# Performance work log

Measured on AMD Instinct MI355X. Metric: run time of the kernel, lower is better.

The kernel has to match this reference:

```python
import jax, jax.numpy as jnp
import numpy as np

K_DIM = 1024
HEADS = 16


def setup_inputs() -> dict:
    key = jax.random.key(0)
    kx, kw1, kb1, kw2, kb2 = jax.random.split(key, 5)
    b, t, k = 4, 2048, K_DIM
    scale = 1.0 / np.sqrt(k)
    x = jax.random.normal(kx, (b, t, k), dtype=jnp.float32)
    # torch nn.Linear params: weight [out, in], bias [out]
    W_qkv = jax.random.normal(kw1, (3 * k, k), dtype=jnp.float32) * scale
    b_qkv = jax.random.normal(kb1, (3 * k,), dtype=jnp.float32) * scale
    W_out = jax.random.normal(kw2, (k, k), dtype=jnp.float32) * scale
    b_out = jax.random.normal(kb2, (k,), dtype=jnp.float32) * scale
    return {"x": x, "W_qkv": W_qkv, "b_qkv": b_qkv, "W_out": W_out, "b_out": b_out}


def reference(x, W_qkv, b_qkv, W_out, b_out):
    b, t, k = x.shape
    h = HEADS
    s = k // h
    # tokqv linear: [b,t,3k]
    kqv = jnp.einsum('btk,ok->bto', x, W_qkv) + b_qkv
    # view [b,t,h,3s] -> transpose -> [b,h,t,3s], then split q,k,v along last dim
    kqv = kqv.reshape(b, t, h, 3 * s).transpose(0, 2, 1, 3)
    q, kk, v = kqv[..., :s], kqv[..., s:2 * s], kqv[..., 2 * s:]
    scores = jnp.einsum('bhqd,bhkd->bhqk', q, kk) / jnp.sqrt(jnp.float32(s * h))  # note: scale uses full k per source (queries.size(-1)=s, but here head dim s)
    # Faithful: original attention scales by sqrt(queries.size(-1)) = sqrt(s)
    scores = jnp.einsum('bhqd,bhkd->bhqk', q, kk) / jnp.sqrt(jnp.float32(s))
    weights = jax.nn.softmax(scores, axis=-1)
    res = jnp.einsum('bhqk,bhkd->bhqd', weights, v)  # [b,h,t,s]
    res = res.transpose(0, 2, 1, 3).reshape(b, t, k)
    return jnp.einsum('btk,ok->bto', res, W_out) + b_out
```

## Files before the change

### kernel.cpp

```cpp
#include <hip/hip_runtime.h>
#include <hip/hip_bf16.h>

typedef float  f32x4  __attribute__((ext_vector_type(4)));
typedef float  f32x8  __attribute__((ext_vector_type(8)));
typedef float  f32x16 __attribute__((ext_vector_type(16)));
typedef __bf16 bf16x8 __attribute__((ext_vector_type(8)));
typedef unsigned short u16x4 __attribute__((ext_vector_type(4)));
typedef unsigned short u16x8 __attribute__((ext_vector_type(8)));
typedef unsigned int   u32x4 __attribute__((ext_vector_type(4)));

#define QSCALE 0.18033688011112042f

__device__ __forceinline__ unsigned short f2bf(float f) {
  __bf16 h = (__bf16)f;
  return __builtin_bit_cast(unsigned short, h);
}

__device__ __forceinline__ f32x4 mfma16(bf16x8 a, bf16x8 b, f32x4 c) {
  return __builtin_amdgcn_mfma_f32_16x16x32_bf16(a, b, c, 0, 0, 0);
}
__device__ __forceinline__ f32x16 mfma32(bf16x8 a, bf16x8 b, f32x16 c) {
  return __builtin_amdgcn_mfma_f32_32x32x16_bf16(a, b, c, 0, 0, 0);
}
__device__ __forceinline__ f32x16 zero16() {
  f32x16 v;
#pragma unroll
  for (int i = 0; i < 16; ++i) v[i] = 0.f;
  return v;
}

typedef const __attribute__((address_space(1))) void* gptr_t;
typedef __attribute__((address_space(3))) void* lptr_t;
__device__ __forceinline__ void gld16(const void* g, void* l) {
  __builtin_amdgcn_global_load_lds((gptr_t)g, (lptr_t)l, 16, 0, 0);
}


__global__ __launch_bounds__(256) void prep_x(const float* __restrict__ x,
                                              unsigned short* __restrict__ A1) {
  const int mb = blockIdx.x >> 5;
  const int kB = blockIdx.x & 31;
#pragma unroll
  for (int ph = 0; ph < 2; ++ph) {
    int c = threadIdx.x + ph * 256;
    int lg = c >> 7, r = c & 127;
    f32x8 v = *(const f32x8*)(x + (size_t)(mb * 128 + r) * 1024 + kB * 32 + lg * 8);
    u16x8 h;
#pragma unroll
    for (int j = 0; j < 8; ++j) h[j] = f2bf(v[j]);
    *(u16x8*)(A1 + (size_t)(mb * 32 + kB) * 4096 + (size_t)c * 8) = h;
  }
}

__global__ __launch_bounds__(256) void prep_w(const float* __restrict__ w,
                                              unsigned short* __restrict__ o) {
  const int rb = blockIdx.x >> 5;
  const int kB = blockIdx.x & 31;
#pragma unroll
  for (int ph = 0; ph < 2; ++ph) {
    int c = threadIdx.x + ph * 256;
    int lg = c >> 7, r = c & 127;
    f32x8 v = *(const f32x8*)(w + (size_t)(rb * 128 + r) * 1024 + kB * 32 + lg * 8);
    u16x8 h;
#pragma unroll
    for (int j = 0; j < 8; ++j) h[j] = f2bf(v[j]);
    *(u16x8*)(o + (size_t)(rb * 32 + kB) * 4096 + (size_t)c * 8) = h;
  }
}

template <int EPI, int MINW>
__global__ __launch_bounds__(256, MINW) void gemm_bt(
    const __bf16* __restrict__ A, const __bf16* __restrict__ B,
    const float* __restrict__ bias, int N, int nbx, int NT,
    unsigned short* __restrict__ q_out, unsigned short* __restrict__ k_out,
    unsigned short* __restrict__ v_out, float* __restrict__ f_out) {
  __shared__ __align__(16) char smem[3 * 16384];
  const int tid = threadIdx.x;
  const int lane = tid & 63;
  const int wave = tid >> 6;
  const int ln = lane & 15, lg = lane >> 4;
  const int wm = wave >> 1;
  const int wn = wave & 1;
  const int bm = blockIdx.x / nbx;
  const int bn = blockIdx.x % nbx;

  f32x4 acc[4][4];
#pragma unroll
  for (int i = 0; i < 4; ++i)
#pragma unroll
    for (int j = 0; j < 4; ++j) acc[i][j] = (f32x4){0.f, 0.f, 0.f, 0.f};

  const __bf16* Asrc = A + ((size_t)bm * NT) * 4096 + tid * 8;
  const __bf16* Bsrc = B + ((size_t)bn * NT) * 4096 + tid * 8;
  const int aoff = lg * 2048 + (wm * 64 + ln) * 16;
  const int boff = 8192 + lg * 2048 + (wn * 64 + ln) * 16;

#define STAGE(slot_, tf_)                                                      \
  do {                                                                         \
    char* d_ = smem + (slot_) * 16384;                                         \
    const __bf16* a_ = Asrc + (size_t)(tf_) * 4096;                            \
    const __bf16* b_ = Bsrc + (size_t)(tf_) * 4096;                            \
    gld16(a_, d_ + tid * 16);                                                  \
    gld16(a_ + 2048, d_ + 4096 + tid * 16);                                    \
    gld16(b_, d_ + 8192 + tid * 16);                                           \
    gld16(b_ + 2048, d_ + 12288 + tid * 16);                                   \
  } while (0)

#define KBODY(t_, scur_, snxt_)                                                \
  do {                                                                         \
    int tf_ = ((t_) + 2 < NT) ? (t_) + 2 : NT - 1;                             \
    STAGE(snxt_, tf_);                                                         \
    const char* ab_ = smem + (scur_) * 16384;                                  \
    bf16x8 af_[4], bq_[4];                                                     \
    _Pragma("unroll") for (int mi = 0; mi < 4; ++mi)                           \
        af_[mi] = *(const bf16x8*)(ab_ + aoff + mi * 256);                     \
    _Pragma("unroll") for (int ni = 0; ni < 4; ++ni)                           \
        bq_[ni] = *(const bf16x8*)(ab_ + boff + ni * 256);                     \
    __builtin_amdgcn_s_setprio(1);                                             \
    _Pragma("unroll") for (int mi = 0; mi < 4; ++mi)                           \
        _Pragma("unroll") for (int ni = 0; ni < 4; ++ni)                       \
            acc[mi][ni] = mfma16(af_[mi], bq_[ni], acc[mi][ni]);               \
    __builtin_amdgcn_s_setprio(0);                                             \
    asm volatile("s_waitcnt vmcnt(4)\n\ts_barrier" ::: "memory");              \
  } while (0)

  STAGE(0, 0);
  STAGE(1, 1);
  asm volatile("s_waitcnt vmcnt(4)\n\ts_barrier" ::: "memory");

  for (int t = 0; t < NT; t += 3) {
    KBODY(t, 0, 2);
    if (t + 1 < NT) KBODY(t + 1, 1, 0);
    if (t + 2 < NT) KBODY(t + 2, 2, 1);
  }
  asm volatile("s_waitcnt vmcnt(0)" ::: "memory");
#undef KBODY
#undef STAGE

#pragma unroll
  for (int mi = 0; mi < 4; ++mi) {
#pragma unroll
    for (int ni = 0; ni < 4; ++ni) {
      int n = bn * 128 + wn * 64 + ni * 16 + ln;
      float bv = bias[n];
#pragma unroll
      for (int j = 0; j < 4; ++j) {
        int m = bm * 128 + wm * 64 + mi * 16 + lg * 4 + j;
        float val = acc[mi][ni][j] + bv;
        if constexpr (EPI == 0) {
          int h = n / 192;
          int r3 = n - h * 192;
          int b = m >> 11;
          int t = m & 2047;
          size_t base = (size_t)(b * 16 + h) << 17;
          if (r3 < 64) {
            q_out[base + ((size_t)t << 6) + r3] = f2bf(val * QSCALE);
          } else if (r3 < 128) {
            int d = r3 - 64;
            size_t off = base + (size_t)(t >> 6) * 4096 +
                         (size_t)((((t >> 5) & 1) << 2) + (d >> 4)) * 512 +
                         ((d >> 3) & 1) * 256 + (t & 31) * 8 + (d & 7);
            k_out[off] = f2bf(val);
          } else {
            int c = r3 - 128;
            size_t off = base + (size_t)(t >> 6) * 4096 +
                         (size_t)(((c >> 5) << 2) + ((t >> 4) & 3)) * 512 +
                         ((t >> 3) & 1) * 256 + (c & 31) * 8 + (t & 7);
            v_out[off] = f2bf(val);
          }
        } else {
          f_out[(size_t)m * N + n] = val;
        }
      }
    }
  }
}

__global__ __launch_bounds__(512, 4) void attn2(
    const __bf16* __restrict__ Q, const __bf16* __restrict__ Kg,
    const __bf16* __restrict__ Vg, unsigned short* __restrict__ res) {
  __shared__ __align__(16) char smem[2 * 32768];
  const int tid = threadIdx.x;
  const int lane = tid & 63;
  const int wq = tid >> 6;
  const int l31 = lane & 31;
  const int hi = lane >> 5;
  const int bh = blockIdx.x & 63;
  const int q0 = (blockIdx.x >> 6) << 8;
  const size_t bh_elem = (size_t)bh << 17;

  const __bf16* Kbh = Kg + bh_elem;
  const __bf16* Vbh = Vg + bh_elem;

  bf16x8 qf[4];
  {
    const __bf16* qrow = Q + bh_elem + ((size_t)(q0 + wq * 32 + l31) << 6) + hi * 8;
#pragma unroll
    for (int ks = 0; ks < 4; ++ks) qf[ks] = *(const bf16x8*)(qrow + ks * 16);
  }
  const u16x8 one8 = {0x3F80, 0x3F80, 0x3F80, 0x3F80,
                      0x3F80, 0x3F80, 0x3F80, 0x3F80};
  const bf16x8 ones = __builtin_bit_cast(bf16x8, one8);

  const f32x16 fz = zero16();
  f32x16 oacc0 = zero16(), oacc1 = zero16(), lacc = zero16();

#define ASTP(s_, p_)                                                           \
  do {                                                                         \
    char* sb_ = smem + (s_) * 32768;                                           \
    const __bf16* k0_ = Kbh + (size_t)(2 * (p_)) * 4096 + tid * 8;             \
    const __bf16* v0_ = Vbh + (size_t)(2 * (p_)) * 4096 + tid * 8;             \
    gld16(k0_, sb_ + tid * 16);                                                \
    gld16(v0_, sb_ + 8192 + tid * 16);                                         \
    gld16(k0_ + 4096, sb_ + 16384 + tid * 16);                                 \
    gld16(v0_ + 4096, sb_ + 24576 + tid * 16);                                 \
  } while (0)

  ASTP(0, 0);
  ASTP(1, 1);
  asm volatile("s_waitcnt vmcnt(4)\n\ts_barrier" ::: "memory");

  const int t2rev = wq & 1;
  for (int pr = 0; pr < 16; ++pr) {
    if (pr >= 1 && pr < 15) ASTP((pr + 1) & 1, pr + 1);

    const char* pbase = smem + (pr & 1) * 32768;
    const int loff = hi * 512 + l31 * 16;

#pragma unroll
    for (int half = 0; half < 2; ++half) {
      const char* kbase = pbase + half * 16384;
      const char* vbase = kbase + 8192;

#pragma unroll
      for (int tt = 0; tt < 2; ++tt) {
        const int t2 = tt ^ t2rev;
        f32x16 s;
        __builtin_amdgcn_s_setprio(1);
        {
          bf16x8 kf0 = *(const bf16x8*)(kbase + (t2 * 4) * 1024 + loff);
          s = mfma32(kf0, qf[0], fz);
        }
#pragma unroll
        for (int ks = 1; ks < 4; ++ks) {
          bf16x8 kf = *(const bf16x8*)(kbase + (t2 * 4 + ks) * 1024 + loff);
          s = mfma32(kf, qf[ks], s);
        }
        __builtin_amdgcn_s_setprio(0);
        float p[16];
#pragma unroll
        for (int r = 0; r < 16; ++r) p[r] = __builtin_amdgcn_exp2f(s[r]);
        unsigned int pk[8];
#pragma unroll
        for (int i = 0; i < 8; ++i)
          pk[i] = ((unsigned int)f2bf(p[2 * i + 1]) << 16) | f2bf(p[2 * i]);
        asm volatile("v_permlane32_swap_b32 %0, %1" : "+v"(pk[0]), "+v"(pk[2]));
        asm volatile("v_permlane32_swap_b32 %0, %1" : "+v"(pk[1]), "+v"(pk[3]));
        asm volatile("v_permlane32_swap_b32 %0, %1" : "+v"(pk[4]), "+v"(pk[6]));
        asm volatile("v_permlane32_swap_b32 %0, %1" : "+v"(pk[5]), "+v"(pk[7]));
        __builtin_amdgcn_s_setprio(1);
#pragma unroll
        for (int ks2 = 0; ks2 < 2; ++ks2) {
          u32x4 bw = {pk[ks2 * 4 + 0], pk[ks2 * 4 + 1],
                      pk[ks2 * 4 + 2], pk[ks2 * 4 + 3]};
          bf16x8 pb = __builtin_bit_cast(bf16x8, bw);
          int kb2 = t2 * 2 + ks2;
          bf16x8 v0 = *(const bf16x8*)(vbase + (kb2) * 1024 + loff);
          bf16x8 v1 = *(const bf16x8*)(vbase + (4 + kb2) * 1024 + loff);
          lacc  = mfma32(ones, pb, lacc);
          oacc0 = mfma32(v0, pb, oacc0);
          oacc1 = mfma32(v1, pb, oacc1);
        }
        __builtin_amdgcn_s_setprio(0);
      }
    }
    asm volatile("s_waitcnt vmcnt(0)\n\ts_barrier" ::: "memory");
  }
#undef ASTP

  float rl = __builtin_amdgcn_rcpf(lacc[0]);
  const int b = bh >> 4, h = bh & 15;
  const int rloc = wq * 32 + l31;
  const int mb = b * 16 + (blockIdx.x >> 6) * 2 + (rloc >> 7);
  const int r = rloc & 127;
  unsigned short* c0 = res + (size_t)(mb * 32 + 2 * h) * 4096 + r * 8 + hi * 4;
#pragma unroll
  for (int g = 0; g < 4; ++g) {
    u16x4 st0, st1;
#pragma unroll
    for (int rr = 0; rr < 4; ++rr) {
      st0[rr] = f2bf(oacc0[g * 4 + rr] * rl);
      st1[rr] = f2bf(oacc1[g * 4 + rr] * rl);
    }
    *(u16x4*)(c0 + g * 1024) = st0;
    *(u16x4*)(c0 + 4096 + g * 1024) = st1;
  }
}

extern "C" void kernel_launch(void* const* d_in, const int* in_sizes, int n_in,
                              void* d_out, int out_size, void* d_ws, size_t ws_size,
                              hipStream_t stream) {
  const float* x    = (const float*)d_in[0];
  const float* Wqkv = (const float*)d_in[1];
  const float* bqkv = (const float*)d_in[2];
  const float* Wout = (const float*)d_in[3];
  const float* bout = (const float*)d_in[4];
  float* out = (float*)d_out;
  char* ws = (char*)d_ws;

  unsigned short* A1 = (unsigned short*)(ws);
  unsigned short* B1 = (unsigned short*)(ws + 50331648);
  unsigned short* Qb = (unsigned short*)(ws + 69206016);
  unsigned short* Kb = (unsigned short*)(ws + 85983232);
  unsigned short* Vb = (unsigned short*)(ws + 102760448);
  unsigned short* Rb = (unsigned short*)(ws + 119537664);
  unsigned short* Wo = (unsigned short*)(ws + 136314880);

  prep_x<<<64 * 32, 256, 0, stream>>>(x, A1);
  prep_w<<<24 * 32, 256, 0, stream>>>(Wqkv, B1);
  prep_w<<<8 * 32, 256, 0, stream>>>(Wout, Wo);

  gemm_bt<0, 3><<<64 * 24, 256, 0, stream>>>((const __bf16*)A1, (const __bf16*)B1,
                                             bqkv, 3072, 24, 32,
                                             Qb, Kb, Vb, nullptr);

  attn2<<<512, 512, 0, stream>>>((const __bf16*)Qb, (const __bf16*)Kb,
                                 (const __bf16*)Vb, Rb);

  gemm_bt<1, 2><<<64 * 8, 256, 0, stream>>>((const __bf16*)Rb, (const __bf16*)Wo,
                                            bout, 1024, 8, 32,
                                            nullptr, nullptr, nullptr, out);
}
```

Before: 180.8 us.

## Restructure GEMM pipeline to double-buffered two-tile stages; use packed bf16 convert

The GEMM main loop changes from a three-slot ring that holds one k-tile per slot to two slots that each hold two k-tiles. Each iteration issues the next pair's loads, computes two k-tiles, then waits for all loads and barriers, so there are half as many barriers per k-step. LDS per block grows to 64 KB and the QKV GEMM launch bound drops from 3 to 2 waves per SIMD, which may lower occupancy and latency hiding. In the attention kernel, packing two floats to bf16 now uses a single v_cvt_pk_bf16_f32 instruction instead of separate converts, shifts and ors.

Result: slower. 185.6 us (+2.7%).

```diff
diff --git a/kernel.cpp b/kernel.cpp
--- a/kernel.cpp
+++ b/kernel.cpp
@@ -68,13 +68,13 @@
   }
 }
 
-template <int EPI, int MINW>
-__global__ __launch_bounds__(256, MINW) void gemm_bt(
+template <int EPI>
+__global__ __launch_bounds__(256, 2) void gemm_bt(
     const __bf16* __restrict__ A, const __bf16* __restrict__ B,
     const float* __restrict__ bias, int N, int nbx, int NT,
     unsigned short* __restrict__ q_out, unsigned short* __restrict__ k_out,
     unsigned short* __restrict__ v_out, float* __restrict__ f_out) {
-  __shared__ __align__(16) char smem[3 * 16384];
+  __shared__ __align__(16) char smem[2 * 32768];
   const int tid = threadIdx.x;
   const int lane = tid & 63;
   const int wave = tid >> 6;
@@ -95,47 +95,49 @@
   const int aoff = lg * 2048 + (wm * 64 + ln) * 16;
   const int boff = 8192 + lg * 2048 + (wn * 64 + ln) * 16;
 
-#define STAGE(slot_, tf_)                                                      \
+#define STAGEP(s_, pf_)                                                        \
   do {                                                                         \
-    char* d_ = smem + (slot_) * 16384;                                         \
-    const __bf16* a_ = Asrc + (size_t)(tf_) * 4096;                            \
-    const __bf16* b_ = Bsrc + (size_t)(tf_) * 4096;                            \
-    gld16(a_, d_ + tid * 16);                                                  \
-    gld16(a_ + 2048, d_ + 4096 + tid * 16);                                    \
-    gld16(b_, d_ + 8192 + tid * 16);                                           \
-    gld16(b_ + 2048, d_ + 12288 + tid * 16);                                   \
+    _Pragma("unroll") for (int h_ = 0; h_ < 2; ++h_) {                         \
+      const __bf16* a_ = Asrc + (size_t)(2 * (pf_) + h_) * 4096;               \
+      const __bf16* b_ = Bsrc + (size_t)(2 * (pf_) + h_) * 4096;               \
+      char* d_ = smem + (s_) * 32768 + h_ * 16384;                             \
+      gld16(a_, d_ + tid * 16);                                                \
+      gld16(a_ + 2048, d_ + 4096 + tid * 16);                                  \
+      gld16(b_, d_ + 8192 + tid * 16);                                         \
+      gld16(b_ + 2048, d_ + 12288 + tid * 16);                                 \
+    }                                                                          \
   } while (0)
 
-#define KBODY(t_, scur_, snxt_)                                                \
-  do {                                                                         \
-    int tf_ = ((t_) + 2 < NT) ? (t_) + 2 : NT - 1;                             \
-    STAGE(snxt_, tf_);                                                         \
-    const char* ab_ = smem + (scur_) * 16384;                                  \
-    bf16x8 af_[4], bq_[4];                                                     \
-    _Pragma("unroll") for (int mi = 0; mi < 4; ++mi)                           \
-        af_[mi] = *(const bf16x8*)(ab_ + aoff + mi * 256);                     \
-    _Pragma("unroll") for (int ni = 0; ni < 4; ++ni)                           \
-        bq_[ni] = *(const bf16x8*)(ab_ + boff + ni * 256);                     \
-    __builtin_amdgcn_s_setprio(1);                                             \
-    _Pragma("unroll") for (int mi = 0; mi < 4; ++mi)                           \
-        _Pragma("unroll") for (int ni = 0; ni < 4; ++ni)                       \
-            acc[mi][ni] = mfma16(af_[mi], bq_[ni], acc[mi][ni]);               \
-    __builtin_amdgcn_s_setprio(0);                                             \
-    asm volatile("s_waitcnt vmcnt(4)\n\ts_barrier" ::: "memory");              \
-  } while (0)
-
-  STAGE(0, 0);
-  STAGE(1, 1);
-  asm volatile("s_waitcnt vmcnt(4)\n\ts_barrier" ::: "memory");
-
-  for (int t = 0; t < NT; t += 3) {
-    KBODY(t, 0, 2);
-    if (t + 1 < NT) KBODY(t + 1, 1, 0);
-    if (t + 2 < NT) KBODY(t + 2, 2, 1);
-  }
-  asm volatile("s_waitcnt vmcnt(0)" ::: "memory");
-#undef KBODY
-#undef STAGE
+  const int NP = NT >> 1;
+
+  STAGEP(0, 0);
+  STAGEP(1, 1);
+  asm volatile("s_waitcnt vmcnt(8)\n\ts_barrier" ::: "memory");
+
+  for (int i = 0; i < NP; ++i) {
+    if (i >= 1 && i < NP - 1) STAGEP((i + 1) & 1, i + 1);
+    const char* sb = smem + (i & 1) * 32768;
+#pragma unroll
+    for (int h = 0; h < 2; ++h) {
+      const char* hb = sb + h * 16384;
+      bf16x8 af_[4], bq_[4];
+#pragma unroll
+      for (int mi = 0; mi < 4; ++mi)
+        af_[mi] = *(const bf16x8*)(hb + aoff + mi * 256);
+#pragma unroll
+      for (int ni = 0; ni < 4; ++ni)
+        bq_[ni] = *(const bf16x8*)(hb + boff + ni * 256);
+      __builtin_amdgcn_s_setprio(1);
+#pragma unroll
+      for (int mi = 0; mi < 4; ++mi)
+#pragma unroll
+        for (int ni = 0; ni < 4; ++ni)
+          acc[mi][ni] = mfma16(af_[mi], bq_[ni], acc[mi][ni]);
+      __builtin_amdgcn_s_setprio(0);
+    }
+    asm volatile("s_waitcnt vmcnt(0)\n\ts_barrier" ::: "memory");
+  }
+#undef STAGEP
 
 #pragma unroll
   for (int mi = 0; mi < 4; ++mi) {
@@ -253,7 +255,8 @@
         unsigned int pk[8];
 #pragma unroll
         for (int i = 0; i < 8; ++i)
-          pk[i] = ((unsigned int)f2bf(p[2 * i + 1]) << 16) | f2bf(p[2 * i]);
+          asm("v_cvt_pk_bf16_f32 %0, %1, %2"
+              : "=v"(pk[i]) : "v"(p[2 * i]), "v"(p[2 * i + 1]));
         asm volatile("v_permlane32_swap_b32 %0, %1" : "+v"(pk[0]), "+v"(pk[2]));
         asm volatile("v_permlane32_swap_b32 %0, %1" : "+v"(pk[1]), "+v"(pk[3]));
         asm volatile("v_permlane32_swap_b32 %0, %1" : "+v"(pk[4]), "+v"(pk[6]));
@@ -320,14 +323,14 @@
   prep_w<<<24 * 32, 256, 0, stream>>>(Wqkv, B1);
   prep_w<<<8 * 32, 256, 0, stream>>>(Wout, Wo);
 
-  gemm_bt<0, 3><<<64 * 24, 256, 0, stream>>>((const __bf16*)A1, (const __bf16*)B1,
-                                             bqkv, 3072, 24, 32,
-                                             Qb, Kb, Vb, nullptr);
+  gemm_bt<0><<<64 * 24, 256, 0, stream>>>((const __bf16*)A1, (const __bf16*)B1,
+                                          bqkv, 3072, 24, 32,
+                                          Qb, Kb, Vb, nullptr);
 
   attn2<<<512, 512, 0, stream>>>((const __bf16*)Qb, (const __bf16*)Kb,
                                  (const __bf16*)Vb, Rb);
 
-  gemm_bt<1, 2><<<64 * 8, 256, 0, stream>>>((const __bf16*)Rb, (const __bf16*)Wo,
-                                            bout, 1024, 8, 32,
-                                            nullptr, nullptr, nullptr, out);
-}
+  gemm_bt<1><<<64 * 8, 256, 0, stream>>>((const __bf16*)Rb, (const __bf16*)Wo,
+                                         bout, 1024, 8, 32,
+                                         nullptr, nullptr, nullptr, out);
+}
```

## Software-pipeline QK/softmax/PV in attention loop and compute row sums on VALU

Applied to the files above, without the earlier changes.

Restructures the inner attention loop into interleaved QK, softmax and PV stages across two score buffers, so the exp/convert work of one tile overlaps with MFMA work on the next. It drops the extra MFMA against an all-ones matrix that computed the softmax denominator, and instead accumulates row sums with VALU adds plus a final cross-half shuffle. Float-to-bf16 packing now uses a single packed convert instruction. The cost is higher register pressure from two live score tiles and packed buffers, and the denominator is summed from fp32 values rather than the rounded bf16 ones.

After: 178.4 us. About the same (-1.3%).

```diff
diff --git a/kernel.cpp b/kernel.cpp
--- a/kernel.cpp
+++ b/kernel.cpp
@@ -198,12 +198,10 @@
 #pragma unroll
     for (int ks = 0; ks < 4; ++ks) qf[ks] = *(const bf16x8*)(qrow + ks * 16);
   }
-  const u16x8 one8 = {0x3F80, 0x3F80, 0x3F80, 0x3F80,
-                      0x3F80, 0x3F80, 0x3F80, 0x3F80};
-  const bf16x8 ones = __builtin_bit_cast(bf16x8, one8);
 
   const f32x16 fz = zero16();
-  f32x16 oacc0 = zero16(), oacc1 = zero16(), lacc = zero16();
+  f32x16 oacc0 = zero16(), oacc1 = zero16();
+  float lsum = 0.f;
 
 #define ASTP(s_, p_)                                                           \
   do {                                                                         \
@@ -216,69 +214,94 @@
     gld16(v0_ + 4096, sb_ + 24576 + tid * 16);                                 \
   } while (0)
 
+#define QK(s_, half_, t2_)                                                     \
+  do {                                                                         \
+    const char* kb_ = pbase + (half_) * 16384;                                 \
+    __builtin_amdgcn_s_setprio(1);                                             \
+    {                                                                          \
+      bf16x8 kf0_ = *(const bf16x8*)(kb_ + ((t2_) * 4) * 1024 + loff);         \
+      s_ = mfma32(kf0_, qf[0], fz);                                            \
+    }                                                                          \
+    _Pragma("unroll") for (int ks = 1; ks < 4; ++ks) {                         \
+      bf16x8 kf_ = *(const bf16x8*)(kb_ + ((t2_) * 4 + ks) * 1024 + loff);     \
+      s_ = mfma32(kf_, qf[ks], s_);                                            \
+    }                                                                          \
+    __builtin_amdgcn_s_setprio(0);                                             \
+  } while (0)
+
+#define SM(pk_, s_)                                                            \
+  do {                                                                         \
+    float p_[16];                                                              \
+    _Pragma("unroll") for (int r = 0; r < 16; ++r)                             \
+        p_[r] = __builtin_amdgcn_exp2f(s_[r]);                                 \
+    _Pragma("unroll") for (int i = 0; i < 8; ++i)                              \
+        asm("v_cvt_pk_bf16_f32 %0, %1, %2"                                     \
+            : "=v"(pk_[i]) : "v"(p_[2 * i]), "v"(p_[2 * i + 1]));              \
+    float sa_ = (p_[0] + p_[1]) + (p_[2] + p_[3]);                             \
+    float sb_ = (p_[4] + p_[5]) + (p_[6] + p_[7]);                             \
+    float sc_ = (p_[8] + p_[9]) + (p_[10] + p_[11]);                           \
+    float sd_ = (p_[12] + p_[13]) + (p_[14] + p_[15]);                         \
+    lsum += (sa_ + sb_) + (sc_ + sd_);                                         \
+    asm volatile("v_permlane32_swap_b32 %0, %1" : "+v"(pk_[0]), "+v"(pk_[2])); \
+    asm volatile("v_permlane32_swap_b32 %0, %1" : "+v"(pk_[1]), "+v"(pk_[3])); \
+    asm volatile("v_permlane32_swap_b32 %0, %1" : "+v"(pk_[4]), "+v"(pk_[6])); \
+    asm volatile("v_permlane32_swap_b32 %0, %1" : "+v"(pk_[5]), "+v"(pk_[7])); \
+  } while (0)
+
+#define PV(pk_, half_, t2_)                                                    \
+  do {                                                                         \
+    const char* vb_ = pbase + (half_) * 16384 + 8192;                          \
+    __builtin_amdgcn_s_setprio(1);                                             \
+    _Pragma("unroll") for (int ks2 = 0; ks2 < 2; ++ks2) {                      \
+      u32x4 bw_ = {pk_[ks2 * 4 + 0], pk_[ks2 * 4 + 1],                         \
+                   pk_[ks2 * 4 + 2], pk_[ks2 * 4 + 3]};                        \
+      bf16x8 pb_ = __builtin_bit_cast(bf16x8, bw_);                            \
+      int kb2_ = (t2_) * 2 + ks2;                                              \
+      bf16x8 v0_ = *(const bf16x8*)(vb_ + kb2_ * 1024 + loff);                 \
+      bf16x8 v1_ = *(const bf16x8*)(vb_ + (4 + kb2_) * 1024 + loff);           \
+      oacc0 = mfma32(v0_, pb_, oacc0);                                         \
+      oacc1 = mfma32(v1_, pb_, oacc1);                                         \
+    }                                                                          \
+    __builtin_amdgcn_s_setprio(0);                                             \
+  } while (0)
+
   ASTP(0, 0);
   ASTP(1, 1);
   asm volatile("s_waitcnt vmcnt(4)\n\ts_barrier" ::: "memory");
 
-  const int t2rev = wq & 1;
+  const int ta = wq & 1;
+  const int tb = 1 - ta;
+  const int loff = hi * 512 + l31 * 16;
+
   for (int pr = 0; pr < 16; ++pr) {
     if (pr >= 1 && pr < 15) ASTP((pr + 1) & 1, pr + 1);
 
     const char* pbase = smem + (pr & 1) * 32768;
-    const int loff = hi * 512 + l31 * 16;
-
-#pragma unroll
-    for (int half = 0; half < 2; ++half) {
-      const char* kbase = pbase + half * 16384;
-      const char* vbase = kbase + 8192;
-
-#pragma unroll
-      for (int tt = 0; tt < 2; ++tt) {
-        const int t2 = tt ^ t2rev;
-        f32x16 s;
-        __builtin_amdgcn_s_setprio(1);
-        {
-          bf16x8 kf0 = *(const bf16x8*)(kbase + (t2 * 4) * 1024 + loff);
-          s = mfma32(kf0, qf[0], fz);
-        }
-#pragma unroll
-        for (int ks = 1; ks < 4; ++ks) {
-          bf16x8 kf = *(const bf16x8*)(kbase + (t2 * 4 + ks) * 1024 + loff);
-          s = mfma32(kf, qf[ks], s);
-        }
-        __builtin_amdgcn_s_setprio(0);
-        float p[16];
-#pragma unroll
-        for (int r = 0; r < 16; ++r) p[r] = __builtin_amdgcn_exp2f(s[r]);
-        unsigned int pk[8];
-#pragma unroll
-        for (int i = 0; i < 8; ++i)
-          pk[i] = ((unsigned int)f2bf(p[2 * i + 1]) << 16) | f2bf(p[2 * i]);
-        asm volatile("v_permlane32_swap_b32 %0, %1" : "+v"(pk[0]), "+v"(pk[2]));
-        asm volatile("v_permlane32_swap_b32 %0, %1" : "+v"(pk[1]), "+v"(pk[3]));
-        asm volatile("v_permlane32_swap_b32 %0, %1" : "+v"(pk[4]), "+v"(pk[6]));
-        asm volatile("v_permlane32_swap_b32 %0, %1" : "+v"(pk[5]), "+v"(pk[7]));
-        __builtin_amdgcn_s_setprio(1);
-#pragma unroll
-        for (int ks2 = 0; ks2 < 2; ++ks2) {
-          u32x4 bw = {pk[ks2 * 4 + 0], pk[ks2 * 4 + 1],
-                      pk[ks2 * 4 + 2], pk[ks2 * 4 + 3]};
-          bf16x8 pb = __builtin_bit_cast(bf16x8, bw);
-          int kb2 = t2 * 2 + ks2;
-          bf16x8 v0 = *(const bf16x8*)(vbase + (kb2) * 1024 + loff);
-          bf16x8 v1 = *(const bf16x8*)(vbase + (4 + kb2) * 1024 + loff);
-          lacc  = mfma32(ones, pb, lacc);
-          oacc0 = mfma32(v0, pb, oacc0);
-          oacc1 = mfma32(v1, pb, oacc1);
-        }
-        __builtin_amdgcn_s_setprio(0);
-      }
-    }
+
+    f32x16 sA, sB;
+    unsigned int pkA[8], pkB[8];
+    QK(sA, 0, ta);
+    SM(pkA, sA);
+    QK(sB, 0, tb);
+    PV(pkA, 0, ta);
+    SM(pkB, sB);
+    QK(sA, 1, ta);
+    PV(pkB, 0, tb);
+    SM(pkA, sA);
+    QK(sB, 1, tb);
+    PV(pkA, 1, ta);
+    SM(pkB, sB);
+    PV(pkB, 1, tb);
+
     asm volatile("s_waitcnt vmcnt(0)\n\ts_barrier" ::: "memory");
   }
+#undef PV
+#undef SM
+#undef QK
 #undef ASTP
 
-  float rl = __builtin_amdgcn_rcpf(lacc[0]);
+  float ltot = lsum + __shfl_xor(lsum, 32, 64);
+  float rl = __builtin_amdgcn_rcpf(ltot);
   const int b = bh >> 4, h = bh & 15;
   const int rloc = wq * 32 + l31;
   const int mb = b * 16 + (blockIdx.x >> 6) * 2 + (rloc >> 7);
```
